# Kernel optimization log

Measured on AMD Instinct MI355X. Metric: run time of the kernel, lower is better.

## Reference

```python
import jax, jax.numpy as jnp
import numpy as np

N_NODES = 100000
N_EDGES = 1000000
IN_F = 64
HID = 64
N_GRAPHS = 1000
HEADS = 4
NOTES = 128
NUM_MPNNS = 4
NUM_CONVS = 2
NUM_LINEARS = 3  # num_hidden_layers=2 -> 3 Linear layers in GIN MLP
EPS_BN = 1e-5


def setup_inputs() -> dict:
    key = jax.random.key(0)
    ks = jax.random.split(key, 16)
    s = 0.05
    x = jax.random.normal(ks[0], (N_NODES, IN_F), dtype=jnp.float32)
    edge_index = jax.random.randint(ks[1], (2, N_EDGES), 0, N_NODES)
    batch = jnp.sort(jax.random.randint(ks[2], (N_NODES,), 0, N_GRAPHS))
    dh = HID // HEADS
    return {
        'x': x,
        'edge_index': edge_index,
        'batch': batch,
        # feature BatchNorm affine params
        'fn_gamma': jnp.ones((IN_F,), jnp.float32),
        'fn_beta': jnp.zeros((IN_F,), jnp.float32),
        # input projection
        'proj_W': jax.random.normal(ks[3], (IN_F, HID), jnp.float32) * s,
        'proj_b': jnp.zeros((HID,), jnp.float32),
        # GIN MLPs: [num_mpnns, num_linears, HID, HID]
        'mlp_W': jax.random.normal(ks[4], (NUM_MPNNS, NUM_LINEARS, HID, HID), jnp.float32) * s,
        'mlp_b': jnp.zeros((NUM_MPNNS, NUM_LINEARS, HID), jnp.float32),
        # per-block conv BatchNorm affine params
        'norm_gamma': jnp.ones((NUM_MPNNS, HID), jnp.float32),
        'norm_beta': jnp.zeros((NUM_MPNNS, HID), jnp.float32),
        # attention readout (PMA-style): learned seed query per head
        'attn_seed': jax.random.normal(ks[5], (HEADS, dh), jnp.float32) * s,
        'attn_Wk': jax.random.normal(ks[6], (HID, HID), jnp.float32) * s,
        'attn_Wv': jax.random.normal(ks[7], (HID, HID), jnp.float32) * s,
        'attn_Wo': jax.random.normal(ks[8], (HID, HID), jnp.float32) * s,
        # notes predictor
        'pred_W': jax.random.normal(ks[9], (HID, NOTES), jnp.float32) * s,
        'pred_b': jnp.zeros((NOTES,), jnp.float32),
    }


def _batchnorm(z, gamma, beta):
    # training-mode BatchNorm1d over the node dimension (biased variance)
    mu = jnp.mean(z, axis=0)
    var = jnp.var(z, axis=0)
    return (z - mu) * jax.lax.rsqrt(var + EPS_BN) * gamma + beta


def reference(x, edge_index, batch, fn_gamma, fn_beta, proj_W, proj_b,
              mlp_W, mlp_b, norm_gamma, norm_beta,
              attn_seed, attn_Wk, attn_Wv, attn_Wo, pred_W, pred_b):
    src, dst = edge_index[0], edge_index[1]

    # feature norm + projection (dropout = identity at inference)
    h = _batchnorm(x, fn_gamma, fn_beta)
    h = jax.nn.relu(h @ proj_W + proj_b)
    residual = h

    # GINConv blocks: h' = MLP((1+eps)*h + sum_{j in N(i)} h_j), eps=0
    for m in range(NUM_MPNNS):
        for _ in range(NUM_CONVS):
            agg = h + jax.ops.segment_sum(h[src], dst, num_segments=N_NODES)
            z = agg
            for l in range(NUM_LINEARS):
                z = z @ mlp_W[m, l] + mlp_b[m, l]
                if l < NUM_LINEARS - 1:
                    z = jax.nn.relu(z)
            z = _batchnorm(z, norm_gamma[m], norm_beta[m])
            h = jax.nn.relu(z)
        h = h + residual
        residual = h

    # attention readout (PMA-style set attention pooling per graph)
    dh = HID // HEADS
    k = (h @ attn_Wk).reshape(N_NODES, HEADS, dh)
    v = (h @ attn_Wv).reshape(N_NODES, HEADS, dh)
    scores = jnp.einsum('nhd,hd->nh', k, attn_seed) / jnp.sqrt(jnp.float32(dh))
    smax = jax.ops.segment_max(scores, batch, num_segments=N_GRAPHS)  # [G,H]
    e = jnp.exp(scores - smax[batch])
    denom = jax.ops.segment_sum(e, batch, num_segments=N_GRAPHS)  # [G,H]
    attn = e / denom[batch]  # [N,H]
    pooled = jax.ops.segment_sum(attn[:, :, None] * v, batch, num_segments=N_GRAPHS)  # [G,H,dh]
    embed = pooled.reshape(N_GRAPHS, HID) @ attn_Wo  # [G, HID]

    logits = embed @ pred_W + pred_b
    return embed, logits
```

## Files before the change

kernel.cpp:

```cpp
#include <hip/hip_runtime.h>

#define LDA 68

typedef __attribute__((ext_vector_type(8))) short bf16x8;
typedef __attribute__((ext_vector_type(4))) float floatx4;

__device__ __forceinline__ unsigned short f2bf(float f)
{
    union { float f; unsigned int u; } v; v.f = f;
    unsigned int r = (v.u + 0x7fffu + ((v.u >> 16) & 1u)) >> 16;
    return (unsigned short)r;
}
__device__ __forceinline__ float bf2f(unsigned short b)
{
    union { unsigned int u; float f; } v; v.u = ((unsigned int)b) << 16;
    return v.f;
}

#define MFMA3(accv, ah, al, bh, bl)                                              \
    accv = __builtin_amdgcn_mfma_f32_16x16x32_bf16(ah, bh, accv, 0, 0, 0);       \
    accv = __builtin_amdgcn_mfma_f32_16x16x32_bf16(al, bh, accv, 0, 0, 0);       \
    accv = __builtin_amdgcn_mfma_f32_16x16x32_bf16(ah, bl, accv, 0, 0, 0);

#define BFRAG(P, n, kc, qd) (*(const bf16x8*)((P) + ((n) << 6) + (kc) * 32 + (qd) * 8))

__device__ __forceinline__ void pack_pair(const float* f, bf16x8& hi, bf16x8& lo)
{
#pragma unroll
    for (int j = 0; j < 8; ++j) {
        unsigned short hb = f2bf(f[j]);
        hi[j] = (short)hb;
        lo[j] = (short)f2bf(f[j] - bf2f(hb));
    }
}


__global__ void k_prep(const float* __restrict__ pW, const float* __restrict__ mlpW,
                       const float* __restrict__ Wv,
                       short* __restrict__ preH, short* __restrict__ preL)
{
    int mat = blockIdx.x;
    const float* Wg = (mat == 0) ? pW : ((mat <= 12) ? mlpW + (size_t)(mat - 1) * 4096 : Wv);
    int t = threadIdx.x;
    short* dh = preH + (size_t)mat * 4096;
    short* dl = preL + (size_t)mat * 4096;
#pragma unroll
    for (int i = 0; i < 16; ++i) {
        int idx = i * 256 + t;
        int k = idx >> 6, n = idx & 63;
        float w = Wg[idx];
        unsigned short hb = f2bf(w);
        dh[n * 64 + k] = (short)hb;
        dl[n * 64 + k] = (short)f2bf(w - bf2f(hb));
    }
}


__global__ void k_count(const int* __restrict__ dst, int* __restrict__ cnt, int E)
{
    for (int e = blockIdx.x * 256 + threadIdx.x; e < E; e += gridDim.x * 256)
        atomicAdd(&cnt[dst[e]], 1);
}

__global__ void k_scan1(const int* __restrict__ cnt, int* __restrict__ bsum, int n)
{
    __shared__ int red[256];
    int t = threadIdx.x;
    int i = blockIdx.x * 256 + t;
    red[t] = (i < n) ? cnt[i] : 0;
    __syncthreads();
    for (int off = 128; off; off >>= 1) {
        if (t < off) red[t] += red[t + off];
        __syncthreads();
    }
    if (t == 0) bsum[blockIdx.x] = red[0];
}

__global__ void k_scan2(const int* __restrict__ bsum, int* __restrict__ boff,
                        int nb, int* __restrict__ rowptrN)
{
    __shared__ int sc[512];
    int t = threadIdx.x;
    int v = (t < nb) ? bsum[t] : 0;
    sc[t] = v;
    __syncthreads();
    for (int off = 1; off < 512; off <<= 1) {
        int u = (t >= off) ? sc[t - off] : 0;
        __syncthreads();
        sc[t] += u;
        __syncthreads();
    }
    if (t < nb) boff[t] = sc[t] - v;
    if (t == nb - 1) *rowptrN = sc[t];
}

__global__ void k_scan3(int* __restrict__ cnt, const int* __restrict__ boff,
                        int* __restrict__ rowptr, int n)
{
    __shared__ int sc[256];
    int t = threadIdx.x;
    int i = blockIdx.x * 256 + t;
    int v = (i < n) ? cnt[i] : 0;
    sc[t] = v;
    __syncthreads();
    for (int off = 1; off < 256; off <<= 1) {
        int u = (t >= off) ? sc[t - off] : 0;
        __syncthreads();
        sc[t] += u;
        __syncthreads();
    }
    if (i < n) {
        rowptr[i] = boff[blockIdx.x] + sc[t] - v;
        cnt[i] = 0;
    }
}

__global__ void k_fill(const int* __restrict__ src, const int* __restrict__ dst,
                       const int* __restrict__ rowptr, int* __restrict__ cursor,
                       int* __restrict__ col, int E)
{
    for (int e = blockIdx.x * 256 + threadIdx.x; e < E; e += gridDim.x * 256) {
        int d = dst[e];
        int p = atomicAdd(&cursor[d], 1);
        col[rowptr[d] + p] = src[e];
    }
}


__global__ void k_xstats(const float* __restrict__ x, float* __restrict__ stats, int N)
{
    __shared__ float rs[256], rq[256];
    int t = threadIdx.x;
    int f = t & 63, rg = t >> 6;
    float s = 0.f, q = 0.f;
    for (int r = blockIdx.x * 4 + rg; r < N; r += gridDim.x * 4) {
        float v = x[(size_t)r * 64 + f];
        s += v; q += v * v;
    }
    rs[rg * 64 + f] = s; rq[rg * 64 + f] = q;
    __syncthreads();
    if (t < 64) {
        float ts = rs[t] + rs[64 + t] + rs[128 + t] + rs[192 + t];
        float tq = rq[t] + rq[64 + t] + rq[128 + t] + rq[192 + t];
        int rep = (blockIdx.x & 3) * 128;
        atomicAdd(&stats[rep + t], ts);
        atomicAdd(&stats[rep + 64 + t], tq);
    }
}

__device__ __forceinline__ void finalize_lds(const float* __restrict__ stats,
                                             const float* __restrict__ gamma,
                                             const float* __restrict__ beta,
                                             float* __restrict__ SS, int t, float invN)
{
    if (t < 64) {
        float su = stats[t] + stats[128 + t] + stats[256 + t] + stats[384 + t];
        float qu = stats[64 + t] + stats[192 + t] + stats[320 + t] + stats[448 + t];
        float mu = su * invN;
        float var = qu * invN - mu * mu;
        float sc = gamma[t] * rsqrtf(var + 1e-5f);
        SS[t] = sc;
        SS[64 + t] = beta[t] - mu * sc;
    }
}


__global__ void __launch_bounds__(256, 4)
k_proj(const float* __restrict__ x, const float* __restrict__ stats,
       const float* __restrict__ fn_g, const float* __restrict__ fn_b,
       const short* __restrict__ WH, const short* __restrict__ WL,
       const float* __restrict__ b,
       float* __restrict__ res, unsigned short* __restrict__ hbh,
       int N, float invN)
{
    __shared__ float ScSh[128];
    __shared__ float BiasSh[64];
    int t = threadIdx.x;
    int wave = t >> 6, lane = t & 63;
    int m = lane & 15, qd = lane >> 4;
    int base = blockIdx.x * 64;
    int nodeA = base + wave * 16 + m;

    finalize_lds(stats, fn_g, fn_b, ScSh, t, invN);
    if (t < 64) BiasSh[t] = b[t];
    __syncthreads();

    int rowc = min(nodeA, N - 1);
    bf16x8 ah[2], al[2];
#pragma unroll
    for (int kc = 0; kc < 2; ++kc) {
        floatx4 x0 = *(const floatx4*)(x + (size_t)rowc * 64 + kc * 32 + qd * 8);
        floatx4 x1 = *(const floatx4*)(x + (size_t)rowc * 64 + kc * 32 + qd * 8 + 4);
        float av[8];
#pragma unroll
        for (int j = 0; j < 8; ++j) {
            int k = kc * 32 + qd * 8 + j;
            float xv = (j < 4) ? x0[j] : x1[j - 4];
            av[j] = xv * ScSh[k] + ScSh[64 + k];
        }
        pack_pair(av, ah[kc], al[kc]);
    }

    floatx4 acc[4];
#pragma unroll
    for (int tt = 0; tt < 4; ++tt) {
        float bv = BiasSh[tt * 16 + m];
        acc[tt] = (floatx4){bv, bv, bv, bv};
    }
#pragma unroll
    for (int kc = 0; kc < 2; ++kc)
#pragma unroll
        for (int tt = 0; tt < 4; ++tt) {
            bf16x8 bh = BFRAG(WH, tt * 16 + m, kc, qd);
            bf16x8 bl = BFRAG(WL, tt * 16 + m, kc, qd);
            MFMA3(acc[tt], ah[kc], al[kc], bh, bl);
        }

#pragma unroll
    for (int tt = 0; tt < 4; ++tt)
#pragma unroll
        for (int r = 0; r < 4; ++r) {
            int node = base + wave * 16 + qd * 4 + r;
            if (node < N) {
                int col = tt * 16 + m;
                float v = fmaxf(acc[tt][r], 0.f);
                res[(size_t)node * 64 + col] = v;
                hbh[(size_t)node * 64 + col] = f2bf(v);
            }
        }
}


__global__ void __launch_bounds__(256, 8)
k_conv(const unsigned short* __restrict__ hbh,
       const int* __restrict__ rowptr, const int* __restrict__ col,
       const short* __restrict__ WH, const short* __restrict__ WL,
       const float* __restrict__ b3,
       float* __restrict__ z, float* __restrict__ stats, int N)
{
    __shared__ __align__(16) float Aint[64 * 68];
    __shared__ float BiasSh[192];
    int t = threadIdx.x;
    int wave = t >> 6, lane = t & 63;
    int m = lane & 15, qd = lane >> 4;
    int base = blockIdx.x * 64;
    float* Aw = Aint + wave * 1088;

    if (t < 192) BiasSh[t] = b3[t];

#pragma unroll 1
    for (int i = 0; i < 16; ++i) {
        int node = base + wave * 16 + i;
        float a = 0.f;
        if (node < N) {
            a = bf2f(hbh[(size_t)node * 64 + lane]);
            int e0 = rowptr[node], e1 = rowptr[node + 1];
            int e = e0;
            for (; e + 8 <= e1; e += 8) {
                int s0 = col[e + 0], s1 = col[e + 1], s2 = col[e + 2], s3 = col[e + 3];
                int s4 = col[e + 4], s5 = col[e + 5], s6 = col[e + 6], s7 = col[e + 7];
                float v0 = bf2f(hbh[(size_t)s0 * 64 + lane]);
                float v1 = bf2f(hbh[(size_t)s1 * 64 + lane]);
                float v2 = bf2f(hbh[(size_t)s2 * 64 + lane]);
                float v3 = bf2f(hbh[(size_t)s3 * 64 + lane]);
                float v4 = bf2f(hbh[(size_t)s4 * 64 + lane]);
                float v5 = bf2f(hbh[(size_t)s5 * 64 + lane]);
                float v6 = bf2f(hbh[(size_t)s6 * 64 + lane]);
                float v7 = bf2f(hbh[(size_t)s7 * 64 + lane]);
                a += ((v0 + v1) + (v2 + v3)) + ((v4 + v5) + (v6 + v7));
            }
            if (e + 4 <= e1) {
                int s0 = col[e + 0], s1 = col[e + 1], s2 = col[e + 2], s3 = col[e + 3];
                a += (bf2f(hbh[(size_t)s0 * 64 + lane]) + bf2f(hbh[(size_t)s1 * 64 + lane]))
                   + (bf2f(hbh[(size_t)s2 * 64 + lane]) + bf2f(hbh[(size_t)s3 * 64 + lane]));
                e += 4;
            }
            if (e + 2 <= e1) {
                a += bf2f(hbh[(size_t)col[e] * 64 + lane]) + bf2f(hbh[(size_t)col[e + 1] * 64 + lane]);
                e += 2;
            }
            if (e < e1) a += bf2f(hbh[(size_t)col[e] * 64 + lane]);
        }
        Aw[i * 68 + lane] = a;
    }
    __syncthreads();

    floatx4 acc[4];

#pragma unroll 1
    for (int l = 0; l < 3; ++l) {
        const short* LH = WH + l * 4096;
        const short* LL = WL + l * 4096;
#pragma unroll
        for (int tt = 0; tt < 4; ++tt) {
            float bv = BiasSh[l * 64 + tt * 16 + m];
            acc[tt] = (floatx4){bv, bv, bv, bv};
        }
#pragma unroll
        for (int kc = 0; kc < 2; ++kc) {
            floatx4 x0 = *(const floatx4*)(Aw + m * 68 + kc * 32 + qd * 8);
            floatx4 x1 = *(const floatx4*)(Aw + m * 68 + kc * 32 + qd * 8 + 4);
            float av[8];
#pragma unroll
            for (int j = 0; j < 8; ++j) av[j] = (j < 4) ? x0[j] : x1[j - 4];
            bf16x8 ah, al;
            pack_pair(av, ah, al);
#pragma unroll
            for (int tt = 0; tt < 4; ++tt) {
                bf16x8 bh = BFRAG(LH, tt * 16 + m, kc, qd);
                bf16x8 bl = BFRAG(LL, tt * 16 + m, kc, qd);
                MFMA3(acc[tt], ah, al, bh, bl);
            }
        }
        if (l < 2) {
            __syncthreads();
#pragma unroll
            for (int tt = 0; tt < 4; ++tt)
#pragma unroll
                for (int r = 0; r < 4; ++r)
                    Aw[(qd * 4 + r) * 68 + tt * 16 + m] = fmaxf(acc[tt][r], 0.f);
            __syncthreads();
        }
    }

#pragma unroll
    for (int tt = 0; tt < 4; ++tt)
#pragma unroll
        for (int r = 0; r < 4; ++r) {
            int node = base + wave * 16 + qd * 4 + r;
            if (node < N)
                z[(size_t)node * 64 + tt * 16 + m] = acc[tt][r];
        }

    __syncthreads();
    float* SW = Aint;
#pragma unroll
    for (int tt = 0; tt < 4; ++tt) {
        float s = 0.f, q = 0.f;
#pragma unroll
        for (int r = 0; r < 4; ++r) {
            int node = base + wave * 16 + qd * 4 + r;
            float v = (node < N) ? acc[tt][r] : 0.f;
            s += v; q += v * v;
        }
        SW[(tt * 16 + m) * 16 + wave * 4 + qd] = s;
        SW[2048 + (tt * 16 + m) * 16 + wave * 4 + qd] = q;
    }
    __syncthreads();
    if (t < 64) {
        float s = 0.f, q = 0.f;
#pragma unroll
        for (int i = 0; i < 16; ++i) { s += SW[t * 16 + i]; q += SW[2048 + t * 16 + i]; }
        int rep = (blockIdx.x & 3) * 128;
        atomicAdd(&stats[rep + t], s);
        atomicAdd(&stats[rep + 64 + t], q);
    }
}


__global__ void k_bnrelu(const float4* __restrict__ z4,
                         const float* __restrict__ stats, const float* __restrict__ gamma,
                         const float* __restrict__ beta,
                         float4* __restrict__ res4,
                         ushort4* __restrict__ hbh4, ushort4* __restrict__ hbl4,
                         int second, int writeLo, int total4, float invN)
{
    __shared__ float SS[128];
    int t = threadIdx.x;
    finalize_lds(stats, gamma, beta, SS, t, invN);
    __syncthreads();
    for (int idx = blockIdx.x * 256 + t; idx < total4; idx += gridDim.x * 256) {
        int c = (idx & 15) << 2;
        float4 v = z4[idx];
        v.x = fmaxf(v.x * SS[c + 0] + SS[64 + c + 0], 0.f);
        v.y = fmaxf(v.y * SS[c + 1] + SS[64 + c + 1], 0.f);
        v.z = fmaxf(v.z * SS[c + 2] + SS[64 + c + 2], 0.f);
        v.w = fmaxf(v.w * SS[c + 3] + SS[64 + c + 3], 0.f);
        if (second) {
            float4 r = res4[idx];
            v.x += r.x; v.y += r.y; v.z += r.z; v.w += r.w;
            res4[idx] = v;
        }
        ushort4 ph;
        ph.x = f2bf(v.x); ph.y = f2bf(v.y); ph.z = f2bf(v.z); ph.w = f2bf(v.w);
        hbh4[idx] = ph;
        if (writeLo) {
            ushort4 pl;
            pl.x = f2bf(v.x - bf2f(ph.x));
            pl.y = f2bf(v.y - bf2f(ph.y));
            pl.z = f2bf(v.z - bf2f(ph.z));
            pl.w = f2bf(v.w - bf2f(ph.w));
            hbl4[idx] = pl;
        }
    }
}


__global__ void __launch_bounds__(256, 4)
k_vs(const unsigned short* __restrict__ hbh, const unsigned short* __restrict__ hbl,
     const short* __restrict__ WH, const short* __restrict__ WL,
     const float* __restrict__ Wk, const float* __restrict__ seed,
     float* __restrict__ v, float* __restrict__ scores, int N)
{
    __shared__ short Sh[16 * 72], Sl[16 * 72];
    int t = threadIdx.x;
    int wave = t >> 6, lane = t & 63;
    int m = lane & 15, qd = lane >> 4;
    int base = blockIdx.x * 64;
    int nodeA = base + wave * 16 + m;

    {
        int k = t >> 2, n = t & 3;
        float s = 0.f;
#pragma unroll
        for (int d = 0; d < 16; ++d) s += Wk[k * 64 + n * 16 + d] * seed[n * 16 + d];
        s *= 0.25f;
        unsigned short hb = f2bf(s);
        Sh[n * 72 + k] = (short)hb;
        Sl[n * 72 + k] = (short)f2bf(s - bf2f(hb));
        unsigned int* Z1 = (unsigned int*)(Sh + 4 * 72);
        unsigned int* Z2 = (unsigned int*)(Sl + 4 * 72);
        for (int idx2 = t; idx2 < 432; idx2 += 256) { Z1[idx2] = 0; Z2[idx2] = 0; }
    }

    bf16x8 ah[2], al[2];
#pragma unroll
    for (int kc = 0; kc < 2; ++kc) {
        ah[kc] = *(const bf16x8*)(hbh + (size_t)nodeA * 64 + kc * 32 + qd * 8);
        al[kc] = *(const bf16x8*)(hbl + (size_t)nodeA * 64 + kc * 32 + qd * 8);
    }
    __syncthreads();

    floatx4 acc[5] = {};
#pragma unroll
    for (int kc = 0; kc < 2; ++kc) {
#pragma unroll
        for (int tt = 0; tt < 4; ++tt) {
            bf16x8 bh = BFRAG(WH, tt * 16 + m, kc, qd);
            bf16x8 bl = BFRAG(WL, tt * 16 + m, kc, qd);
            MFMA3(acc[tt], ah[kc], al[kc], bh, bl);
        }
        bf16x8 sh = *(const bf16x8*)(Sh + m * 72 + kc * 32 + qd * 8);
        bf16x8 sl = *(const bf16x8*)(Sl + m * 72 + kc * 32 + qd * 8);
        MFMA3(acc[4], ah[kc], al[kc], sh, sl);
    }

#pragma unroll
    for (int tt = 0; tt < 4; ++tt)
#pragma unroll
        for (int r = 0; r < 4; ++r) {
            int node = base + wave * 16 + qd * 4 + r;
            if (node < N)
                v[(size_t)node * 64 + tt * 16 + m] = acc[tt][r];
        }
    if (m < 4) {
#pragma unroll
        for (int r = 0; r < 4; ++r) {
            int node = base + wave * 16 + qd * 4 + r;
            if (node < N) scores[(size_t)node * 4 + m] = acc[4][r];
        }
    }
}


__global__ void k_tail(const float4* __restrict__ scores4, const float* __restrict__ v,
                       const int* __restrict__ batch,
                       const float* __restrict__ Wo, const float* __restrict__ predW,
                       const float* __restrict__ predb,
                       float* __restrict__ emb, float* __restrict__ logits, int N)
{
    int g = blockIdx.x;
    int t = threadIdx.x;
    __shared__ int sb[2];
    __shared__ float4 rmax[256];
    __shared__ float racc[256];
    __shared__ float resum[16];
    __shared__ float pooledSh[64];
    __shared__ float embSh[64];
    if (t < 2) {
        int target = g + t;
        int lo = 0, hi = N;
        while (lo < hi) {
            int mid = (lo + hi) >> 1;
            if (batch[mid] < target) lo = mid + 1; else hi = mid;
        }
        sb[t] = lo;
    }
    __syncthreads();
    int s = sb[0], e = sb[1];
    if (s >= e) {
        if (t < 64) pooledSh[t] = 0.f;
    } else {
        float4 m = make_float4(-1e30f, -1e30f, -1e30f, -1e30f);
        for (int i = s + t; i < e; i += 256) {
            float4 sc = scores4[i];
            m.x = fmaxf(m.x, sc.x); m.y = fmaxf(m.y, sc.y);
            m.z = fmaxf(m.z, sc.z); m.w = fmaxf(m.w, sc.w);
        }
        rmax[t] = m;
        __syncthreads();
        for (int off = 128; off; off >>= 1) {
            if (t < off) {
                float4 a = rmax[t], b = rmax[t + off];
                a.x = fmaxf(a.x, b.x); a.y = fmaxf(a.y, b.y);
                a.z = fmaxf(a.z, b.z); a.w = fmaxf(a.w, b.w);
                rmax[t] = a;
            }
            __syncthreads();
        }
        float4 smax = rmax[0];
        int rg = t >> 6, f = t & 63, hh = f >> 4;
        float mx = (hh == 0) ? smax.x : ((hh == 1) ? smax.y : ((hh == 2) ? smax.z : smax.w));
        float acc = 0.f, es = 0.f;
        for (int i = s + rg; i < e; i += 4) {
            float4 sc = scores4[i];
            float scl = (hh == 0) ? sc.x : ((hh == 1) ? sc.y : ((hh == 2) ? sc.z : sc.w));
            float ev = __expf(scl - mx);
            acc += ev * v[(size_t)i * 64 + f];
            if ((f & 15) == 0) es += ev;
        }
        racc[rg * 64 + f] = acc;
        if ((f & 15) == 0) resum[rg * 4 + hh] = es;
        __syncthreads();
        if (t < 64) {
            float tot = racc[t] + racc[64 + t] + racc[128 + t] + racc[192 + t];
            int h2 = t >> 4;
            float den = resum[h2] + resum[4 + h2] + resum[8 + h2] + resum[12 + h2];
            pooledSh[t] = tot / den;
        }
    }
    __syncthreads();

    if (t < 64) {
        float s2 = 0.f;
#pragma unroll 4
        for (int k = 0; k < 64; ++k) s2 = fmaf(pooledSh[k], Wo[k * 64 + t], s2);
        embSh[t] = s2;
        emb[(size_t)g * 64 + t] = s2;
    }
    __syncthreads();

    if (t < 128) {
        float s2 = predb[t];
#pragma unroll 4
        for (int k = 0; k < 64; ++k) s2 = fmaf(embSh[k], predW[k * 128 + t], s2);
        logits[(size_t)g * 128 + t] = s2;
    }
}


extern "C" void kernel_launch(void* const* d_in, const int* in_sizes, int n_in,
                              void* d_out, int out_size, void* d_ws, size_t ws_size,
                              hipStream_t stream)
{
    const float* x     = (const float*)d_in[0];
    const int*   eidx  = (const int*)d_in[1];
    const int*   batch = (const int*)d_in[2];
    const float* fn_g  = (const float*)d_in[3];
    const float* fn_b  = (const float*)d_in[4];
    const float* pW    = (const float*)d_in[5];
    const float* pb    = (const float*)d_in[6];
    const float* mlpW  = (const float*)d_in[7];
    const float* mlpb  = (const float*)d_in[8];
    const float* ngm   = (const float*)d_in[9];
    const float* nbt   = (const float*)d_in[10];
    const float* seed  = (const float*)d_in[11];
    const float* Wk    = (const float*)d_in[12];
    const float* Wv    = (const float*)d_in[13];
    const float* Wo    = (const float*)d_in[14];
    const float* predW = (const float*)d_in[15];
    const float* predb = (const float*)d_in[16];

    const int N = 100000, E = 1000000, G = 1000;
    const int* srcv = eidx;
    const int* dstv = eidx + E;

    char* w = (char*)d_ws;
    auto alloc = [&](size_t bytes) {
        char* p = w;
        w += (bytes + 255) & ~(size_t)255;
        return p;
    };
    const size_t NPAD = 100032;
    float*          res  = (float*)alloc(NPAD * 64 * 4);
    float*          z    = (float*)alloc(NPAD * 64 * 4);
    unsigned short* hbh  = (unsigned short*)alloc(NPAD * 64 * 2);
    unsigned short* hbl  = (unsigned short*)alloc(NPAD * 64 * 2);
    short* preH = (short*)alloc(14 * 4096 * 2);
    short* preL = (short*)alloc(14 * 4096 * 2);
    int*   rowptr = (int*)alloc((size_t)(N + 1) * 4);
    int*   cnt    = (int*)alloc((size_t)N * 4);
    int*   col    = (int*)alloc((size_t)E * 4);
    int*   bsum   = (int*)alloc(512 * 4);
    int*   boff   = (int*)alloc(512 * 4);
    float* stats  = (float*)alloc(9 * 512 * 4);
    float* scores = (float*)alloc(NPAD * 4 * 4);

    float* emb    = (float*)d_out;
    float* logits = (float*)d_out + G * 64;

    const int NB = (N + 63) / 64;
    const int NBS = (N + 255) / 256;
    const float invN = 1.f / (float)N;

    hipMemsetAsync(cnt, 0, (size_t)N * 4, stream);
    hipMemsetAsync(stats, 0, 9 * 512 * 4, stream);
    k_prep<<<14, 256, 0, stream>>>(pW, mlpW, Wv, preH, preL);
    k_count<<<1024, 256, 0, stream>>>(dstv, cnt, E);
    k_scan1<<<NBS, 256, 0, stream>>>(cnt, bsum, N);
    k_scan2<<<1, 512, 0, stream>>>(bsum, boff, NBS, rowptr + N);
    k_scan3<<<NBS, 256, 0, stream>>>(cnt, boff, rowptr, N);
    k_fill<<<1024, 256, 0, stream>>>(srcv, dstv, rowptr, cnt, col, E);

    k_xstats<<<512, 256, 0, stream>>>(x, stats, N);
    k_proj<<<NB, 256, 0, stream>>>(x, stats, fn_g, fn_b, preH, preL, pb, res, hbh, N, invN);

    for (int m = 0; m < 4; ++m)
        for (int c = 0; c < 2; ++c) {
            int sidx = 1 + m * 2 + c;
            int mat = 1 + m * 3;
            k_conv<<<NB, 256, 0, stream>>>(hbh, rowptr, col,
                                           preH + (size_t)mat * 4096, preL + (size_t)mat * 4096,
                                           mlpb + (size_t)m * 3 * 64,
                                           z, stats + (size_t)sidx * 512, N);
            int last = (m == 3 && c == 1) ? 1 : 0;
            k_bnrelu<<<2048, 256, 0, stream>>>(
                (const float4*)z,
                stats + (size_t)sidx * 512, ngm + m * 64, nbt + m * 64,
                (float4*)res, (ushort4*)hbh, (ushort4*)hbl,
                (c == 1) ? 1 : 0, last, N * 16, invN);
        }

    float* vbuf = z;
    k_vs<<<NB, 256, 0, stream>>>(hbh, hbl, preH + 13 * 4096, preL + 13 * 4096,
                                 Wk, seed, vbuf, scores, N);
    k_tail<<<G, 256, 0, stream>>>((const float4*)scores, vbuf, batch,
                                  Wo, predW, predb, emb, logits, N);
}
```

Before: 993.6 us.

## Partition CSR by source range so gather passes stay cache-resident

Each destination's edge list is split into four buckets by source-node range (25000 nodes each), built through an expanded count/scan/fill with 4N counters. The conv gather then walks all nodes of a block once per source range. The aim is to keep the gathered bf16 feature rows of one range (about 3.2 MB) hot in L2 across the concurrently running blocks. The cost is a larger CSR build with a 400K-entry scan, more rowptr loads, and shorter per-bucket edge loops that give less memory-level parallelism.

New measurement: 1.372 ms. 38.1% more time.

```diff
diff --git a/kernel.cpp b/kernel.cpp
--- a/kernel.cpp
+++ b/kernel.cpp
@@ -1,6 +1,7 @@
 #include <hip/hip_runtime.h>
 
-#define LDA 68
+#define NR 4
+#define RSZ 25000
 
 typedef __attribute__((ext_vector_type(8))) short bf16x8;
 typedef __attribute__((ext_vector_type(4))) float floatx4;
@@ -56,20 +57,23 @@
 }
 
 
-__global__ void k_count(const int* __restrict__ dst, int* __restrict__ cnt, int E)
-{
-    for (int e = blockIdx.x * 256 + threadIdx.x; e < E; e += gridDim.x * 256)
-        atomicAdd(&cnt[dst[e]], 1);
+__global__ void k_count(const int* __restrict__ src, const int* __restrict__ dst,
+                        int* __restrict__ cnt, int E)
+{
+    for (int e = blockIdx.x * 256 + threadIdx.x; e < E; e += gridDim.x * 256) {
+        int s = src[e], d = dst[e];
+        atomicAdd(&cnt[d * NR + s / RSZ], 1);
+    }
 }
 
 __global__ void k_scan1(const int* __restrict__ cnt, int* __restrict__ bsum, int n)
 {
-    __shared__ int red[256];
-    int t = threadIdx.x;
-    int i = blockIdx.x * 256 + t;
+    __shared__ int red[1024];
+    int t = threadIdx.x;
+    int i = blockIdx.x * 1024 + t;
     red[t] = (i < n) ? cnt[i] : 0;
     __syncthreads();
-    for (int off = 128; off; off >>= 1) {
+    for (int off = 512; off; off >>= 1) {
         if (t < off) red[t] += red[t + off];
         __syncthreads();
     }
@@ -97,13 +101,13 @@
 __global__ void k_scan3(int* __restrict__ cnt, const int* __restrict__ boff,
                         int* __restrict__ rowptr, int n)
 {
-    __shared__ int sc[256];
-    int t = threadIdx.x;
-    int i = blockIdx.x * 256 + t;
+    __shared__ int sc[1024];
+    int t = threadIdx.x;
+    int i = blockIdx.x * 1024 + t;
     int v = (i < n) ? cnt[i] : 0;
     sc[t] = v;
     __syncthreads();
-    for (int off = 1; off < 256; off <<= 1) {
+    for (int off = 1; off < 1024; off <<= 1) {
         int u = (t >= off) ? sc[t - off] : 0;
         __syncthreads();
         sc[t] += u;
@@ -120,9 +124,10 @@
                        int* __restrict__ col, int E)
 {
     for (int e = blockIdx.x * 256 + threadIdx.x; e < E; e += gridDim.x * 256) {
-        int d = dst[e];
-        int p = atomicAdd(&cursor[d], 1);
-        col[rowptr[d] + p] = src[e];
+        int s = src[e], d = dst[e];
+        int idx = d * NR + s / RSZ;
+        int p = atomicAdd(&cursor[idx], 1);
+        col[rowptr[idx] + p] = s;
     }
 }
 
@@ -252,9 +257,19 @@
     for (int i = 0; i < 16; ++i) {
         int node = base + wave * 16 + i;
         float a = 0.f;
-        if (node < N) {
-            a = bf2f(hbh[(size_t)node * 64 + lane]);
-            int e0 = rowptr[node], e1 = rowptr[node + 1];
+        if (node < N) a = bf2f(hbh[(size_t)node * 64 + lane]);
+        Aw[i * 68 + lane] = a;
+    }
+
+#pragma unroll 1
+    for (int p = 0; p < NR; ++p) {
+#pragma unroll 1
+        for (int i = 0; i < 16; ++i) {
+            int node = base + wave * 16 + i;
+            if (node >= N) continue;
+            int e0 = rowptr[node * NR + p], e1 = rowptr[node * NR + p + 1];
+            if (e0 == e1) continue;
+            float a = 0.f;
             int e = e0;
             for (; e + 8 <= e1; e += 8) {
                 int s0 = col[e + 0], s1 = col[e + 1], s2 = col[e + 2], s3 = col[e + 3];
@@ -280,8 +295,8 @@
                 e += 2;
             }
             if (e < e1) a += bf2f(hbh[(size_t)col[e] * 64 + lane]);
-        }
-        Aw[i * 68 + lane] = a;
+            Aw[i * 68 + lane] += a;
+        }
     }
     __syncthreads();
 
@@ -588,8 +603,8 @@
     unsigned short* hbl  = (unsigned short*)alloc(NPAD * 64 * 2);
     short* preH = (short*)alloc(14 * 4096 * 2);
     short* preL = (short*)alloc(14 * 4096 * 2);
-    int*   rowptr = (int*)alloc((size_t)(N + 1) * 4);
-    int*   cnt    = (int*)alloc((size_t)N * 4);
+    int*   rowptr = (int*)alloc(((size_t)NR * N + 1) * 4);
+    int*   cnt    = (int*)alloc((size_t)NR * N * 4);
     int*   col    = (int*)alloc((size_t)E * 4);
     int*   bsum   = (int*)alloc(512 * 4);
     int*   boff   = (int*)alloc(512 * 4);
@@ -600,16 +615,17 @@
     float* logits = (float*)d_out + G * 64;
 
     const int NB = (N + 63) / 64;
-    const int NBS = (N + 255) / 256;
+    const int NRN = NR * N;
+    const int NBS = (NRN + 1023) / 1024;
     const float invN = 1.f / (float)N;
 
-    hipMemsetAsync(cnt, 0, (size_t)N * 4, stream);
+    hipMemsetAsync(cnt, 0, (size_t)NRN * 4, stream);
     hipMemsetAsync(stats, 0, 9 * 512 * 4, stream);
     k_prep<<<14, 256, 0, stream>>>(pW, mlpW, Wv, preH, preL);
-    k_count<<<1024, 256, 0, stream>>>(dstv, cnt, E);
-    k_scan1<<<NBS, 256, 0, stream>>>(cnt, bsum, N);
-    k_scan2<<<1, 512, 0, stream>>>(bsum, boff, NBS, rowptr + N);
-    k_scan3<<<NBS, 256, 0, stream>>>(cnt, boff, rowptr, N);
+    k_count<<<1024, 256, 0, stream>>>(srcv, dstv, cnt, E);
+    k_scan1<<<NBS, 1024, 0, stream>>>(cnt, bsum, NRN);
+    k_scan2<<<1, 512, 0, stream>>>(bsum, boff, NBS, rowptr + NRN);
+    k_scan3<<<NBS, 1024, 0, stream>>>(cnt, boff, rowptr, NRN);
     k_fill<<<1024, 256, 0, stream>>>(srcv, dstv, rowptr, cnt, col, E);
 
     k_xstats<<<512, 256, 0, stream>>>(x, stats, N);
```

## Fold BatchNorm+ReLU into next conv gather and into value/score kernel

Applied to the files above, without the earlier changes.

The first conv of each block now writes its MLP output as bf16 and skips the separate BN+ReLU pass. The second conv finalizes the first conv's statistics and applies the BN affine plus ReLU to every gathered neighbor value on the fly. The last block's BN+ReLU and residual add are folded into the value/score kernel, which reads fp32 z and res directly, so the hi/lo bf16 split buffers are no longer written. This removes several full-tensor elementwise passes and launches. In exchange the gather does extra FMA/max work per edge element and the intermediate z is kept at bf16 precision.

Measured after the change: 960.4 us. 1.03x faster.

```diff
diff --git a/kernel.cpp b/kernel.cpp
--- a/kernel.cpp
+++ b/kernel.cpp
@@ -1,6 +1,4 @@
 #include <hip/hip_runtime.h>
-
-#define LDA 68
 
 typedef __attribute__((ext_vector_type(8))) short bf16x8;
 typedef __attribute__((ext_vector_type(4))) float floatx4;
@@ -232,14 +230,18 @@
 
 
 __global__ void __launch_bounds__(256, 8)
-k_conv(const unsigned short* __restrict__ hbh,
+k_conv(const unsigned short* __restrict__ gsrc,
        const int* __restrict__ rowptr, const int* __restrict__ col,
        const short* __restrict__ WH, const short* __restrict__ WL,
        const float* __restrict__ b3,
-       float* __restrict__ z, float* __restrict__ stats, int N)
+       const float* __restrict__ pstats, const float* __restrict__ gamma,
+       const float* __restrict__ beta,
+       float* __restrict__ zout, unsigned short* __restrict__ zbout,
+       float* __restrict__ stats, int N, int mode, float invN)
 {
     __shared__ __align__(16) float Aint[64 * 68];
     __shared__ float BiasSh[192];
+    __shared__ float SS[128];
     int t = threadIdx.x;
     int wave = t >> 6, lane = t & 63;
     int m = lane & 15, qd = lane >> 4;
@@ -247,39 +249,49 @@
     float* Aw = Aint + wave * 1088;
 
     if (t < 192) BiasSh[t] = b3[t];
+    if (mode) {
+        finalize_lds(pstats, gamma, beta, SS, t, invN);
+    } else if (t < 128) {
+        SS[t] = (t < 64) ? 1.f : 0.f;
+    }
+    __syncthreads();
+    float sc = SS[lane], sh = SS[64 + lane];
 
 #pragma unroll 1
     for (int i = 0; i < 16; ++i) {
         int node = base + wave * 16 + i;
         float a = 0.f;
         if (node < N) {
-            a = bf2f(hbh[(size_t)node * 64 + lane]);
+            a = fmaxf(bf2f(gsrc[(size_t)node * 64 + lane]) * sc + sh, 0.f);
             int e0 = rowptr[node], e1 = rowptr[node + 1];
             int e = e0;
             for (; e + 8 <= e1; e += 8) {
                 int s0 = col[e + 0], s1 = col[e + 1], s2 = col[e + 2], s3 = col[e + 3];
                 int s4 = col[e + 4], s5 = col[e + 5], s6 = col[e + 6], s7 = col[e + 7];
-                float v0 = bf2f(hbh[(size_t)s0 * 64 + lane]);
-                float v1 = bf2f(hbh[(size_t)s1 * 64 + lane]);
-                float v2 = bf2f(hbh[(size_t)s2 * 64 + lane]);
-                float v3 = bf2f(hbh[(size_t)s3 * 64 + lane]);
-                float v4 = bf2f(hbh[(size_t)s4 * 64 + lane]);
-                float v5 = bf2f(hbh[(size_t)s5 * 64 + lane]);
-                float v6 = bf2f(hbh[(size_t)s6 * 64 + lane]);
-                float v7 = bf2f(hbh[(size_t)s7 * 64 + lane]);
+                float v0 = fmaxf(bf2f(gsrc[(size_t)s0 * 64 + lane]) * sc + sh, 0.f);
+                float v1 = fmaxf(bf2f(gsrc[(size_t)s1 * 64 + lane]) * sc + sh, 0.f);
+                float v2 = fmaxf(bf2f(gsrc[(size_t)s2 * 64 + lane]) * sc + sh, 0.f);
+                float v3 = fmaxf(bf2f(gsrc[(size_t)s3 * 64 + lane]) * sc + sh, 0.f);
+                float v4 = fmaxf(bf2f(gsrc[(size_t)s4 * 64 + lane]) * sc + sh, 0.f);
+                float v5 = fmaxf(bf2f(gsrc[(size_t)s5 * 64 + lane]) * sc + sh, 0.f);
+                float v6 = fmaxf(bf2f(gsrc[(size_t)s6 * 64 + lane]) * sc + sh, 0.f);
+                float v7 = fmaxf(bf2f(gsrc[(size_t)s7 * 64 + lane]) * sc + sh, 0.f);
                 a += ((v0 + v1) + (v2 + v3)) + ((v4 + v5) + (v6 + v7));
             }
             if (e + 4 <= e1) {
                 int s0 = col[e + 0], s1 = col[e + 1], s2 = col[e + 2], s3 = col[e + 3];
-                a += (bf2f(hbh[(size_t)s0 * 64 + lane]) + bf2f(hbh[(size_t)s1 * 64 + lane]))
-                   + (bf2f(hbh[(size_t)s2 * 64 + lane]) + bf2f(hbh[(size_t)s3 * 64 + lane]));
+                a += (fmaxf(bf2f(gsrc[(size_t)s0 * 64 + lane]) * sc + sh, 0.f)
+                    + fmaxf(bf2f(gsrc[(size_t)s1 * 64 + lane]) * sc + sh, 0.f))
+                   + (fmaxf(bf2f(gsrc[(size_t)s2 * 64 + lane]) * sc + sh, 0.f)
+                    + fmaxf(bf2f(gsrc[(size_t)s3 * 64 + lane]) * sc + sh, 0.f));
                 e += 4;
             }
             if (e + 2 <= e1) {
-                a += bf2f(hbh[(size_t)col[e] * 64 + lane]) + bf2f(hbh[(size_t)col[e + 1] * 64 + lane]);
+                a += fmaxf(bf2f(gsrc[(size_t)col[e] * 64 + lane]) * sc + sh, 0.f)
+                   + fmaxf(bf2f(gsrc[(size_t)col[e + 1] * 64 + lane]) * sc + sh, 0.f);
                 e += 2;
             }
-            if (e < e1) a += bf2f(hbh[(size_t)col[e] * 64 + lane]);
+            if (e < e1) a += fmaxf(bf2f(gsrc[(size_t)col[e] * 64 + lane]) * sc + sh, 0.f);
         }
         Aw[i * 68 + lane] = a;
     }
@@ -328,8 +340,11 @@
 #pragma unroll
         for (int r = 0; r < 4; ++r) {
             int node = base + wave * 16 + qd * 4 + r;
-            if (node < N)
-                z[(size_t)node * 64 + tt * 16 + m] = acc[tt][r];
+            if (node < N) {
+                size_t off = (size_t)node * 64 + tt * 16 + m;
+                if (mode) zout[off] = acc[tt][r];
+                else      zbout[off] = f2bf(acc[tt][r]);
+            }
         }
 
     __syncthreads();
@@ -361,9 +376,8 @@
 __global__ void k_bnrelu(const float4* __restrict__ z4,
                          const float* __restrict__ stats, const float* __restrict__ gamma,
                          const float* __restrict__ beta,
-                         float4* __restrict__ res4,
-                         ushort4* __restrict__ hbh4, ushort4* __restrict__ hbl4,
-                         int second, int writeLo, int total4, float invN)
+                         float4* __restrict__ res4, ushort4* __restrict__ hbh4,
+                         int total4, float invN)
 {
     __shared__ float SS[128];
     int t = threadIdx.x;
@@ -372,36 +386,28 @@
     for (int idx = blockIdx.x * 256 + t; idx < total4; idx += gridDim.x * 256) {
         int c = (idx & 15) << 2;
         float4 v = z4[idx];
-        v.x = fmaxf(v.x * SS[c + 0] + SS[64 + c + 0], 0.f);
-        v.y = fmaxf(v.y * SS[c + 1] + SS[64 + c + 1], 0.f);
-        v.z = fmaxf(v.z * SS[c + 2] + SS[64 + c + 2], 0.f);
-        v.w = fmaxf(v.w * SS[c + 3] + SS[64 + c + 3], 0.f);
-        if (second) {
-            float4 r = res4[idx];
-            v.x += r.x; v.y += r.y; v.z += r.z; v.w += r.w;
-            res4[idx] = v;
-        }
+        float4 r = res4[idx];
+        v.x = fmaxf(v.x * SS[c + 0] + SS[64 + c + 0], 0.f) + r.x;
+        v.y = fmaxf(v.y * SS[c + 1] + SS[64 + c + 1], 0.f) + r.y;
+        v.z = fmaxf(v.z * SS[c + 2] + SS[64 + c + 2], 0.f) + r.z;
+        v.w = fmaxf(v.w * SS[c + 3] + SS[64 + c + 3], 0.f) + r.w;
+        res4[idx] = v;
         ushort4 ph;
         ph.x = f2bf(v.x); ph.y = f2bf(v.y); ph.z = f2bf(v.z); ph.w = f2bf(v.w);
         hbh4[idx] = ph;
-        if (writeLo) {
-            ushort4 pl;
-            pl.x = f2bf(v.x - bf2f(ph.x));
-            pl.y = f2bf(v.y - bf2f(ph.y));
-            pl.z = f2bf(v.z - bf2f(ph.z));
-            pl.w = f2bf(v.w - bf2f(ph.w));
-            hbl4[idx] = pl;
-        }
     }
 }
 
 
 __global__ void __launch_bounds__(256, 4)
-k_vs(const unsigned short* __restrict__ hbh, const unsigned short* __restrict__ hbl,
-     const short* __restrict__ WH, const short* __restrict__ WL,
-     const float* __restrict__ Wk, const float* __restrict__ seed,
-     float* __restrict__ v, float* __restrict__ scores, int N)
-{
+k_bnvs(const float* __restrict__ z, const float* __restrict__ res,
+       const float* __restrict__ stats, const float* __restrict__ gamma,
+       const float* __restrict__ beta,
+       const short* __restrict__ WH, const short* __restrict__ WL,
+       const float* __restrict__ Wk, const float* __restrict__ seed,
+       float* __restrict__ v, float* __restrict__ scores, int N, float invN)
+{
+    __shared__ float ScSh[128];
     __shared__ short Sh[16 * 72], Sl[16 * 72];
     int t = threadIdx.x;
     int wave = t >> 6, lane = t & 63;
@@ -409,6 +415,7 @@
     int base = blockIdx.x * 64;
     int nodeA = base + wave * 16 + m;
 
+    finalize_lds(stats, gamma, beta, ScSh, t, invN);
     {
         int k = t >> 2, n = t & 3;
         float s = 0.f;
@@ -422,14 +429,26 @@
         unsigned int* Z2 = (unsigned int*)(Sl + 4 * 72);
         for (int idx2 = t; idx2 < 432; idx2 += 256) { Z1[idx2] = 0; Z2[idx2] = 0; }
     }
-
+    __syncthreads();
+
+    int rowc = min(nodeA, N - 1);
     bf16x8 ah[2], al[2];
 #pragma unroll
     for (int kc = 0; kc < 2; ++kc) {
-        ah[kc] = *(const bf16x8*)(hbh + (size_t)nodeA * 64 + kc * 32 + qd * 8);
-        al[kc] = *(const bf16x8*)(hbl + (size_t)nodeA * 64 + kc * 32 + qd * 8);
-    }
-    __syncthreads();
+        floatx4 z0 = *(const floatx4*)(z + (size_t)rowc * 64 + kc * 32 + qd * 8);
+        floatx4 z1 = *(const floatx4*)(z + (size_t)rowc * 64 + kc * 32 + qd * 8 + 4);
+        floatx4 r0 = *(const floatx4*)(res + (size_t)rowc * 64 + kc * 32 + qd * 8);
+        floatx4 r1 = *(const floatx4*)(res + (size_t)rowc * 64 + kc * 32 + qd * 8 + 4);
+        float av[8];
+#pragma unroll
+        for (int j = 0; j < 8; ++j) {
+            int k = kc * 32 + qd * 8 + j;
+            float zv = (j < 4) ? z0[j] : z1[j - 4];
+            float rv = (j < 4) ? r0[j] : r1[j - 4];
+            av[j] = fmaxf(zv * ScSh[k] + ScSh[64 + k], 0.f) + rv;
+        }
+        pack_pair(av, ah[kc], al[kc]);
+    }
 
     floatx4 acc[5] = {};
 #pragma unroll
@@ -585,7 +604,7 @@
     float*          res  = (float*)alloc(NPAD * 64 * 4);
     float*          z    = (float*)alloc(NPAD * 64 * 4);
     unsigned short* hbh  = (unsigned short*)alloc(NPAD * 64 * 2);
-    unsigned short* hbl  = (unsigned short*)alloc(NPAD * 64 * 2);
+    unsigned short* zb   = (unsigned short*)alloc(NPAD * 64 * 2);
     short* preH = (short*)alloc(14 * 4096 * 2);
     short* preL = (short*)alloc(14 * 4096 * 2);
     int*   rowptr = (int*)alloc((size_t)(N + 1) * 4);
@@ -615,25 +634,30 @@
     k_xstats<<<512, 256, 0, stream>>>(x, stats, N);
     k_proj<<<NB, 256, 0, stream>>>(x, stats, fn_g, fn_b, preH, preL, pb, res, hbh, N, invN);
 
-    for (int m = 0; m < 4; ++m)
-        for (int c = 0; c < 2; ++c) {
-            int sidx = 1 + m * 2 + c;
-            int mat = 1 + m * 3;
-            k_conv<<<NB, 256, 0, stream>>>(hbh, rowptr, col,
-                                           preH + (size_t)mat * 4096, preL + (size_t)mat * 4096,
-                                           mlpb + (size_t)m * 3 * 64,
-                                           z, stats + (size_t)sidx * 512, N);
-            int last = (m == 3 && c == 1) ? 1 : 0;
+    for (int m = 0; m < 4; ++m) {
+        int mat = 1 + m * 3;
+        const short* WH = preH + (size_t)mat * 4096;
+        const short* WL = preL + (size_t)mat * 4096;
+        const float* b3 = mlpb + (size_t)m * 3 * 64;
+        float* st0 = stats + (size_t)(1 + m * 2) * 512;
+        float* st1 = stats + (size_t)(2 + m * 2) * 512;
+
+        k_conv<<<NB, 256, 0, stream>>>(hbh, rowptr, col, WH, WL, b3,
+                                       nullptr, nullptr, nullptr,
+                                       nullptr, zb, st0, N, 0, invN);
+        k_conv<<<NB, 256, 0, stream>>>(zb, rowptr, col, WH, WL, b3,
+                                       st0, ngm + m * 64, nbt + m * 64,
+                                       z, nullptr, st1, N, 1, invN);
+        if (m < 3)
             k_bnrelu<<<2048, 256, 0, stream>>>(
-                (const float4*)z,
-                stats + (size_t)sidx * 512, ngm + m * 64, nbt + m * 64,
-                (float4*)res, (ushort4*)hbh, (ushort4*)hbl,
-                (c == 1) ? 1 : 0, last, N * 16, invN);
-        }
+                (const float4*)z, st1, ngm + m * 64, nbt + m * 64,
+                (float4*)res, (ushort4*)hbh, N * 16, invN);
+    }
 
     float* vbuf = z;
-    k_vs<<<NB, 256, 0, stream>>>(hbh, hbl, preH + 13 * 4096, preL + 13 * 4096,
-                                 Wk, seed, vbuf, scores, N);
+    k_bnvs<<<NB, 256, 0, stream>>>(z, res, stats + 8 * 512, ngm + 192, nbt + 192,
+                                   preH + 13 * 4096, preL + 13 * 4096,
+                                   Wk, seed, vbuf, scores, N, invN);
     k_tail<<<G, 256, 0, stream>>>((const float4*)scores, vbuf, batch,
                                   Wo, predW, predb, emb, logits, N);
 }
```
